# Optimization experiments

Measured on AMD Instinct MI355X. Metric: run time of the kernel, lower is better.

The kernel has to match this reference:

```python
import jax, jax.numpy as jnp
import numpy as np

EMBED_DIM = 1024
NUM_HEADS = 16
HEAD_DIM = EMBED_DIM // NUM_HEADS
B, T = 4, 1024
NEG = -1.0e9
LN_EPS = 1e-5


def setup_inputs() -> dict:
    key = jax.random.key(0)
    ks = jax.random.split(key, 13)
    s = 1.0 / np.sqrt(EMBED_DIM)
    return {
        "query": jax.random.normal(ks[0], (B, T, EMBED_DIM), jnp.float32),
        "key": jax.random.normal(ks[1], (B, T, EMBED_DIM), jnp.float32),
        "value": jax.random.normal(ks[2], (B, T, EMBED_DIM), jnp.float32),
        "mask": jax.random.randint(ks[3], (B, 1, T, T), 0, 2, jnp.int32),
        "Wq": jax.random.normal(ks[4], (EMBED_DIM, EMBED_DIM), jnp.float32) * s,
        "bq": jnp.zeros((EMBED_DIM,), jnp.float32),
        "Wk": jax.random.normal(ks[5], (EMBED_DIM, EMBED_DIM), jnp.float32) * s,
        "bk": jnp.zeros((EMBED_DIM,), jnp.float32),
        "Wv": jax.random.normal(ks[6], (EMBED_DIM, EMBED_DIM), jnp.float32) * s,
        "bv": jnp.zeros((EMBED_DIM,), jnp.float32),
        "Wo": jax.random.normal(ks[7], (EMBED_DIM, EMBED_DIM), jnp.float32) * s,
        "bo": jnp.zeros((EMBED_DIM,), jnp.float32),
        "gamma": jnp.ones((EMBED_DIM,), jnp.float32),
        "beta": jnp.zeros((EMBED_DIM,), jnp.float32),
    }


def _split_heads(x):
    # (B, T, E) -> (B, H, T, D)
    b, t, _ = x.shape
    return x.reshape(b, t, NUM_HEADS, HEAD_DIM).transpose(0, 2, 1, 3)


def _mha(query, key, value, mask, Wq, bq, Wk, bk, Wv, bv, Wo, bo, gamma, beta,
         temperature=1.0):
    q = _split_heads(query @ Wq.T + bq)
    k = _split_heads(key @ Wk.T + bk)
    v = _split_heads(value @ Wv.T + bv)
    # scores: (B, H, T, T)
    scale = jnp.sqrt(jnp.float32(HEAD_DIM)) * temperature
    scores = jnp.einsum("bhqd,bhkd->bhqk", q, k) / scale
    scores = jnp.where(mask == 0, NEG, scores)
    scores = scores - jnp.max(scores, axis=-1, keepdims=True)
    # temperature >= 0.01 in this config, so the low-temperature hard-cutoff
    # branch is skipped (matches torch's Python-level `if temperature < 0.01`).
    scores = jnp.nan_to_num(scores, nan=0.0, posinf=1.0e9, neginf=-1.0e9)
    attn = jax.nn.softmax(scores, axis=-1)
    # eval mode: dropout is identity (self.training is False)
    out = jnp.einsum("bhqk,bhkd->bhqd", attn, v)  # (B, H, T, D)
    out = out.transpose(0, 2, 1, 3).reshape(query.shape[0], query.shape[1], EMBED_DIM)
    out = out @ Wo.T + bo
    # layer norm over embed_dim
    mu = jnp.mean(out, axis=-1, keepdims=True)
    var = jnp.mean(jnp.square(out - mu), axis=-1, keepdims=True)
    out = (out - mu) * jax.lax.rsqrt(var + LN_EPS) * gamma + beta
    return out


def reference(query, key, value, mask, Wq, bq, Wk, bk, Wv, bv, Wo, bo, gamma, beta):
    return _mha(query, key, value, mask, Wq, bq, Wk, bk, Wv, bv, Wo, bo, gamma, beta)
```

## Files before the change

### kernel.cpp

```cpp
#include <hip/hip_runtime.h>
#include <cmath>

#define T_SEQ 1024
#define EMB   1024
#define NH    16
#define HD    64
#define NB    4
#define BQ    64
#define BK    64

#define QSCALE 0.18033688011112042f
#define BIAS2  -1.44269504e9f

using frag8   = __attribute__((ext_vector_type(8))) short;
using f32x4   = __attribute__((ext_vector_type(4))) float;
using short4v = __attribute__((ext_vector_type(4))) short;
using short8v = __attribute__((ext_vector_type(8))) short;

__device__ inline short f2bf(float f) {
    union { float f; unsigned u; } x; x.f = f;
    unsigned r = (x.u + 0x7FFFu + ((x.u >> 16) & 1u)) >> 16;
    return (short)r;
}
__device__ inline float bf2f(unsigned short u) {
    union { unsigned u; float f; } x; x.u = ((unsigned)u) << 16;
    return x.f;
}
__device__ inline int cvt_pk_bf16(float lo, float hi) {
    int r;
    asm("v_cvt_pk_bf16_f32 %0, %1, %2" : "=v"(r) : "v"(lo), "v"(hi));
    return r;
}

__device__ inline void glds16(const short* g, short* l) {
    __builtin_amdgcn_global_load_lds(
        (const __attribute__((address_space(1))) void*)g,
        (__attribute__((address_space(3))) void*)l, 16, 0, 0);
}

struct ConvArgs { const float* src[7]; short* dst[7]; int n8[7]; };

__global__ __launch_bounds__(256) void convert_bf16(ConvArgs a) {
    const int y = blockIdx.y;
    const int t = blockIdx.x * 256 + threadIdx.x;
    if (t >= a.n8[y]) return;
    const float4* s = (const float4*)a.src[y];
    const float4 v0 = s[t * 2], v1 = s[t * 2 + 1];
    short8v o;
    o[0] = f2bf(v0.x); o[1] = f2bf(v0.y); o[2] = f2bf(v0.z); o[3] = f2bf(v0.w);
    o[4] = f2bf(v1.x); o[5] = f2bf(v1.y); o[6] = f2bf(v1.z); o[7] = f2bf(v1.w);
    *(short8v*)&a.dst[y][t * 8] = o;
}

__global__ __launch_bounds__(256) void convert_mask(
    const int* __restrict__ mask, short* __restrict__ dst)
{
    const int wave = threadIdx.x >> 6, lane = threadIdx.x & 63;
    const int tile = blockIdx.x * 4 + wave;
    const int bb   = tile >> 12;
    const int q16  = (tile >> 6) & 63;
    const int k16  = tile & 63;
    const int qrow = lane >> 2;
    const int col4 = (lane & 3) * 4;
    const int4 mv = *(const int4*)&mask[((size_t)bb * T_SEQ + q16 * 16 + qrow) * T_SEQ
                                        + k16 * 16 + col4];
    const short BB = f2bf(BIAS2);
    short4v o;
    o[0] = mv.x ? (short)0 : BB;
    o[1] = mv.y ? (short)0 : BB;
    o[2] = mv.z ? (short)0 : BB;
    o[3] = mv.w ? (short)0 : BB;
    *(short4v*)&dst[(size_t)tile * 256 + qrow * 16 + col4] = o;
}

struct GemmB { const short* A; const short* W; const float* bias; short* out; float scale; };
struct QkvArgs { GemmB g[3]; };

template <int MODE>
__device__ inline void gemm_core(short* __restrict__ As,
                                 short* __restrict__ Bs,
                                 const short* __restrict__ A,
                                 const short* __restrict__ W,
                                 const float* __restrict__ bias,
                                 float scale,
                                 short* __restrict__ outS,
                                 float* __restrict__ outF,
                                 int m0, int n0)
{
    const int tid  = threadIdx.x;
    const int wave = tid >> 6;
    const int lane = tid & 63;
    const int quad = lane >> 4;
    const int lm   = lane & 15;
    const int wr   = wave >> 1;
    const int wc   = wave & 1;
    const int K    = EMB;

    const int G0 = wave * 64 + lane, G1 = G0 + 256;
    const short* aSrc0 = A + (size_t)(m0 + (G0 >> 2)) * K + (G0 & 3) * 8;
    const short* aSrc1 = A + (size_t)(m0 + (G1 >> 2)) * K + (G1 & 3) * 8;
    const short* bSrc0 = W + (size_t)(n0 + (G0 >> 2)) * K + (G0 & 3) * 8;
    const short* bSrc1 = W + (size_t)(n0 + (G1 >> 2)) * K + (G1 & 3) * 8;
    short* aDst0 = As + wave * 512;
    short* aDst1 = As + 2048 + wave * 512;
    short* bDst0 = Bs + wave * 512;
    short* bDst1 = Bs + 2048 + wave * 512;

    f32x4 acc[4][4];
#pragma unroll
    for (int i = 0; i < 4; ++i)
#pragma unroll
        for (int j = 0; j < 4; ++j) acc[i][j] = (f32x4){0.f, 0.f, 0.f, 0.f};

    for (int kk = 0; kk < K; kk += 64) {
        __syncthreads();
        glds16(aSrc0 + kk,      aDst0);
        glds16(aSrc1 + kk,      aDst1);
        glds16(bSrc0 + kk,      bDst0);
        glds16(bSrc1 + kk,      bDst1);
        glds16(aSrc0 + kk + 32, aDst0 + 4096);
        glds16(aSrc1 + kk + 32, aDst1 + 4096);
        glds16(bSrc0 + kk + 32, bDst0 + 4096);
        glds16(bSrc1 + kk + 32, bDst1 + 4096);
        __syncthreads();

#pragma unroll
        for (int p = 0; p < 2; ++p) {
            frag8 aF[4], bF[4];
#pragma unroll
            for (int i = 0; i < 4; ++i)
                aF[i] = *(const frag8*)&As[p * 4096 + (wr * 64 + i * 16 + lm) * 32 + quad * 8];
#pragma unroll
            for (int j = 0; j < 4; ++j)
                bF[j] = *(const frag8*)&Bs[p * 4096 + (wc * 64 + j * 16 + lm) * 32 + quad * 8];
#pragma unroll
            for (int i = 0; i < 4; ++i)
#pragma unroll
                for (int j = 0; j < 4; ++j)
                    acc[i][j] = __builtin_amdgcn_mfma_f32_16x16x32_bf16(
                        aF[i], bF[j], acc[i][j], 0, 0, 0);
        }
    }

#pragma unroll
    for (int i = 0; i < 4; ++i)
#pragma unroll
        for (int j = 0; j < 4; ++j) {
            const int n = n0 + wc * 64 + j * 16 + lm;
            const float bv = bias[n];
#pragma unroll
            for (int rr = 0; rr < 4; ++rr) {
                const int m = m0 + wr * 64 + i * 16 + quad * 4 + rr;
                const float val = (acc[i][j][rr] + bv) * scale;
                if (MODE == 0) {
                    outF[((size_t)(m >> 4) * 64 + (n >> 4)) * 256 +
                         rr * 64 + quad * 16 + lm] = val;
                } else {
                    const int bb = m >> 10, tt = m & 1023;
                    const int h = n >> 6,  d  = n & 63;
                    const size_t bh = (size_t)bb * NH + h;
                    if (MODE == 1) {
                        outS[((bh * 64 + (tt >> 4)) * 8 + (d >> 3)) * 128 +
                             (tt & 15) * 8 + (d & 7)] = f2bf(val);
                    } else {
                        outS[((((bh * 16 + (tt >> 6)) * 2 + ((tt >> 5) & 1)) * 4 +
                              (d >> 4)) * 4 + ((tt >> 2) & 3)) * 128 +
                             (d & 15) * 8 + (((tt & 16) >> 2) | (tt & 3))] = f2bf(val);
                    }
                }
            }
        }
}

__global__ __launch_bounds__(256, 4) void gemm_qkv(QkvArgs args) {
    __shared__ short As[2 * 128 * 32];
    __shared__ short Bs[2 * 128 * 32];
    const int id = blockIdx.x + 8 * blockIdx.y + 256 * blockIdx.z;
    const int a  = id & 7;
    const int k2 = id >> 3;
    const int nb = k2 & 7;
    const int c  = k2 >> 3;
    const int pair = a * 12 + c;
    const int mb = pair & 31;
    const int zb = pair >> 5;
    const GemmB g = args.g[zb];
    if (zb < 2) gemm_core<1>(As, Bs, g.A, g.W, g.bias, g.scale, g.out, nullptr, mb * 128, nb * 128);
    else        gemm_core<2>(As, Bs, g.A, g.W, g.bias, g.scale, g.out, nullptr, mb * 128, nb * 128);
}

__global__ __launch_bounds__(256, 4) void gemm_wo(const short* __restrict__ A,
                                                  const short* __restrict__ W,
                                                  const float* __restrict__ bias,
                                                  float* __restrict__ out) {
    __shared__ short As[2 * 128 * 32];
    __shared__ short Bs[2 * 128 * 32];
    const int id = blockIdx.x + 8 * blockIdx.y;
    const int a  = id & 7;
    const int k2 = id >> 3;
    const int nb = k2 & 7;
    const int c  = k2 >> 3;
    const int mb = a * 4 + c;
    gemm_core<0>(As, Bs, A, W, bias, 1.0f, nullptr, out, mb * 128, nb * 128);
}

__global__ __launch_bounds__(512, 4) void flash_attn_mfma(
    const short* __restrict__ qf_, const short* __restrict__ kf_,
    const short* __restrict__ vf_, const short* __restrict__ mf_,
    short* __restrict__ out)
{
    __shared__ short KV[4][4096];

    const int tid  = threadIdx.x;
    const int wave = tid >> 6;
    const int lane = tid & 63;
    const int quad = lane >> 4;
    const int lm   = lane & 15;
    const int wq   = wave & 3;
    const int wk   = wave >> 2;

    const int id  = blockIdx.x;
    const int xcd = id & 7;
    const int idx = id >> 3;
    const int bh_i = xcd * 8 + (idx >> 4);
    const int b  = bh_i >> 4, h = bh_i & 15;
    const int q0 = (idx & 15) * BQ;
    const size_t bh = (size_t)bh_i;

    const int  sbuf  = wave >> 1;
    const int  shalf = (wave & 1) * 2048;
    const short* sb = ((sbuf < 2) ? kf_ : vf_) + bh * 65536
                      + (size_t)(sbuf & 1) * 32768 + shalf + lane * 8;
    short* dstb = &KV[sbuf][shalf];

    const short* qb_ = qf_ + (bh * 64 + (q0 >> 4) + wq) * 1024;
    const frag8 qfa = *(const frag8*)&qb_[(quad * 16 + lm) * 8];
    const frag8 qfb = *(const frag8*)&qb_[((quad + 4) * 16 + lm) * 8];

    const short* mrow = mf_ + ((size_t)b * 64 + (q0 >> 4) + wq) * (64 * 256)
                        + lm * 16 + quad * 4;

    union { int i[4]; frag8 f; } ones;
    ones.i[0] = ones.i[1] = ones.i[2] = ones.i[3] = 0x3F803F80;

    f32x4 of[4];
#pragma unroll
    for (int dc = 0; dc < 4; ++dc) of[dc] = (f32x4){0.f, 0.f, 0.f, 0.f};
    f32x4 ls = (f32x4){0.f, 0.f, 0.f, 0.f};

    for (int kt = 0; kt < 8; ++kt) {
        const int kt2 = wk * 8 + kt;

        __syncthreads();
#pragma unroll
        for (int it = 0; it < 4; ++it)
            glds16(sb + kt * 4096 + it * 512, dstb + it * 512);

        short4v mb[4];
#pragma unroll
        for (int kc = 0; kc < 4; ++kc)
            mb[kc] = *(const short4v*)&mrow[(kt2 * 4 + kc) * 256];
        __syncthreads();

        f32x4 s[4];
#pragma unroll
        for (int kc = 0; kc < 4; ++kc) {
            const short* kb = &KV[wk][kc * 1024];
            const frag8 kfa = *(const frag8*)&kb[(quad * 16 + lm) * 8];
            const frag8 kfb = *(const frag8*)&kb[((quad + 4) * 16 + lm) * 8];
            f32x4 a = (f32x4){ bf2f((unsigned short)mb[kc][0]),
                               bf2f((unsigned short)mb[kc][1]),
                               bf2f((unsigned short)mb[kc][2]),
                               bf2f((unsigned short)mb[kc][3]) };
            a = __builtin_amdgcn_mfma_f32_16x16x32_bf16(kfa, qfa, a, 0, 0, 0);
            a = __builtin_amdgcn_mfma_f32_16x16x32_bf16(kfb, qfb, a, 0, 0, 0);
            s[kc] = a;
        }

#pragma unroll
        for (int kc = 0; kc < 4; ++kc) {
            s[kc][0] = exp2f(s[kc][0]); s[kc][1] = exp2f(s[kc][1]);
            s[kc][2] = exp2f(s[kc][2]); s[kc][3] = exp2f(s[kc][3]);
        }

        union { int i[4]; frag8 f; } ua, ub;
        ua.i[0] = cvt_pk_bf16(s[0][0], s[0][1]);
        ua.i[1] = cvt_pk_bf16(s[0][2], s[0][3]);
        ua.i[2] = cvt_pk_bf16(s[1][0], s[1][1]);
        ua.i[3] = cvt_pk_bf16(s[1][2], s[1][3]);
        ub.i[0] = cvt_pk_bf16(s[2][0], s[2][1]);
        ub.i[1] = cvt_pk_bf16(s[2][2], s[2][3]);
        ub.i[2] = cvt_pk_bf16(s[3][0], s[3][1]);
        ub.i[3] = cvt_pk_bf16(s[3][2], s[3][3]);

        __builtin_amdgcn_s_setprio(1);
#pragma unroll
        for (int dc = 0; dc < 4; ++dc) {
            const frag8 v0 = *(const frag8*)&KV[2 + wk][(dc * 4 + quad) * 128 + lm * 8];
            const frag8 v1 = *(const frag8*)&KV[2 + wk][((4 + dc) * 4 + quad) * 128 + lm * 8];
            of[dc] = __builtin_amdgcn_mfma_f32_16x16x32_bf16(v0, ua.f, of[dc], 0, 0, 0);
            of[dc] = __builtin_amdgcn_mfma_f32_16x16x32_bf16(v1, ub.f, of[dc], 0, 0, 0);
        }
        ls = __builtin_amdgcn_mfma_f32_16x16x32_bf16(ones.f, ua.f, ls, 0, 0, 0);
        ls = __builtin_amdgcn_mfma_f32_16x16x32_bf16(ones.f, ub.f, ls, 0, 0, 0);
        __builtin_amdgcn_s_setprio(0);
    }

    float* Osh = (float*)&KV[0][0];
    __syncthreads();
    if (wk) {
#pragma unroll
        for (int c = 0; c < 16; ++c) Osh[(wq * 17 + c) * 64 + lane] = of[c >> 2][c & 3];
        Osh[(wq * 17 + 16) * 64 + lane] = ls[0];
    }
    __syncthreads();
    if (!wk) {
#pragma unroll
        for (int c = 0; c < 16; ++c) of[c >> 2][c & 3] += Osh[(wq * 17 + c) * 64 + lane];
        const float lsum = ls[0] + Osh[(wq * 17 + 16) * 64 + lane];
        const float inv = 1.0f / lsum;

        short* ob = out + ((size_t)b * T_SEQ + q0 + wq * 16 + lm) * EMB + h * HD;
#pragma unroll
        for (int dc = 0; dc < 4; ++dc) {
            short4v o4;
#pragma unroll
            for (int rr = 0; rr < 4; ++rr) o4[rr] = f2bf(of[dc][rr] * inv);
            *(short4v*)&ob[dc * 16 + quad * 4] = o4;
        }
    }
}

__global__ __launch_bounds__(256) void layernorm_k(
    const float* __restrict__ x, const float* __restrict__ gamma,
    const float* __restrict__ beta, float* __restrict__ out)
{
    __shared__ float ws1[4], ws2[4];
    const int tid = threadIdx.x;
    const int row = blockIdx.x;
    const int m16 = row >> 4, rr = row & 3, qd = (row >> 2) & 3;

    const float4 v = *(const float4*)&x[((size_t)m16 * 64 + (tid >> 2)) * 256 +
                                        rr * 64 + qd * 16 + (tid & 3) * 4];
    float s  = v.x + v.y + v.z + v.w;
    float ss = v.x * v.x + v.y * v.y + v.z * v.z + v.w * v.w;
#pragma unroll
    for (int off = 32; off > 0; off >>= 1) {
        s  += __shfl_down(s, off);
        ss += __shfl_down(ss, off);
    }
    if ((tid & 63) == 0) { ws1[tid >> 6] = s; ws2[tid >> 6] = ss; }
    __syncthreads();
    if (tid == 0) {
        const float a = ws1[0] + ws1[1] + ws1[2] + ws1[3];
        const float bsum = ws2[0] + ws2[1] + ws2[2] + ws2[3];
        const float mu = a * (1.0f / EMB);
        const float var = bsum * (1.0f / EMB) - mu * mu;
        ws1[0] = mu;
        ws2[0] = rsqrtf(var + 1e-5f);
    }
    __syncthreads();
    const float mu = ws1[0], rstd = ws2[0];

    const float4 g = *(const float4*)&gamma[tid * 4];
    const float4 bt = *(const float4*)&beta[tid * 4];
    float4 r;
    r.x = (v.x - mu) * rstd * g.x + bt.x;
    r.y = (v.y - mu) * rstd * g.y + bt.y;
    r.z = (v.z - mu) * rstd * g.z + bt.z;
    r.w = (v.w - mu) * rstd * g.w + bt.w;
    *(float4*)&out[(size_t)row * EMB + tid * 4] = r;
}

extern "C" void kernel_launch(void* const* d_in, const int* in_sizes, int n_in,
                              void* d_out, int out_size, void* d_ws, size_t ws_size,
                              hipStream_t stream) {
    const float* query = (const float*)d_in[0];
    const float* key_i = (const float*)d_in[1];
    const float* value = (const float*)d_in[2];
    const int*   mask  = (const int*)d_in[3];
    const float* Wq = (const float*)d_in[4];
    const float* bq = (const float*)d_in[5];
    const float* Wk = (const float*)d_in[6];
    const float* bk = (const float*)d_in[7];
    const float* Wv = (const float*)d_in[8];
    const float* bv = (const float*)d_in[9];
    const float* Wo = (const float*)d_in[10];
    const float* bo = (const float*)d_in[11];
    const float* gamma = (const float*)d_in[12];
    const float* beta  = (const float*)d_in[13];

    const size_t SZ = (size_t)NB * T_SEQ * EMB;
    const size_t WZ = (size_t)EMB * EMB;
    short* sws = (short*)d_ws;
    short* q_bf  = sws;
    short* k_bf  = sws + SZ;
    short* v_bf  = sws + 2 * SZ;
    short* w_bf  = sws + 3 * SZ;
    short* qh    = sws + 4 * SZ;
    short* kh    = sws + 5 * SZ;
    short* vh    = sws + 6 * SZ;
    short* maskb = sws + 7 * SZ;
    short* attnb = q_bf;
    float* projb = (float*)(sws + SZ);

    ConvArgs ca;
    ca.src[0] = query; ca.dst[0] = q_bf;          ca.n8[0] = (int)(SZ / 8);
    ca.src[1] = key_i; ca.dst[1] = k_bf;          ca.n8[1] = (int)(SZ / 8);
    ca.src[2] = value; ca.dst[2] = v_bf;          ca.n8[2] = (int)(SZ / 8);
    ca.src[3] = Wq;    ca.dst[3] = w_bf;          ca.n8[3] = (int)(WZ / 8);
    ca.src[4] = Wk;    ca.dst[4] = w_bf + WZ;     ca.n8[4] = (int)(WZ / 8);
    ca.src[5] = Wv;    ca.dst[5] = w_bf + 2 * WZ; ca.n8[5] = (int)(WZ / 8);
    ca.src[6] = Wo;    ca.dst[6] = w_bf + 3 * WZ; ca.n8[6] = (int)(WZ / 8);
    convert_bf16<<<dim3((SZ / 8 + 255) / 256, 7), 256, 0, stream>>>(ca);

    convert_mask<<<dim3(NB * 64 * 64 / 4), 256, 0, stream>>>(mask, maskb);

    QkvArgs qa;
    qa.g[0] = { q_bf, w_bf,          bq, qh, QSCALE };
    qa.g[1] = { k_bf, w_bf + WZ,     bk, kh, 1.0f };
    qa.g[2] = { v_bf, w_bf + 2 * WZ, bv, vh, 1.0f };
    gemm_qkv<<<dim3(EMB / 128, NB * T_SEQ / 128, 3), 256, 0, stream>>>(qa);

    flash_attn_mfma<<<dim3(T_SEQ / BQ * NH * NB), 512, 0, stream>>>(qh, kh, vh, maskb, attnb);

    gemm_wo<<<dim3(EMB / 128, NB * T_SEQ / 128), 256, 0, stream>>>(
        attnb, w_bf + 3 * WZ, bo, projb);

    layernorm_k<<<dim3(NB * T_SEQ), 256, 0, stream>>>(projb, gamma, beta, (float*)d_out);
}
```

Measured before the change: 249.6 us.

## Double-buffer K/V shared tiles and prefetch mask in flash attention

New measurement: 244.1 us. 2.2% less time.

```diff
diff --git a/kernel.cpp b/kernel.cpp
--- a/kernel.cpp
+++ b/kernel.cpp
@@ -208,7 +208,7 @@
     const short* __restrict__ vf_, const short* __restrict__ mf_,
     short* __restrict__ out)
 {
-    __shared__ short KV[4][4096];
+    __shared__ short KV[2][4][4096];
 
     const int tid  = threadIdx.x;
     const int wave = tid >> 6;
@@ -230,7 +230,6 @@
     const int  shalf = (wave & 1) * 2048;
     const short* sb = ((sbuf < 2) ? kf_ : vf_) + bh * 65536
                       + (size_t)(sbuf & 1) * 32768 + shalf + lane * 8;
-    short* dstb = &KV[sbuf][shalf];
 
     const short* qb_ = qf_ + (bh * 64 + (q0 >> 4) + wq) * 1024;
     const frag8 qfa = *(const frag8*)&qb_[(quad * 16 + lm) * 8];
@@ -247,30 +246,43 @@
     for (int dc = 0; dc < 4; ++dc) of[dc] = (f32x4){0.f, 0.f, 0.f, 0.f};
     f32x4 ls = (f32x4){0.f, 0.f, 0.f, 0.f};
 
+#pragma unroll
+    for (int it = 0; it < 4; ++it)
+        glds16(sb + it * 512, &KV[0][sbuf][shalf + it * 512]);
+    short4v mb[4];
+#pragma unroll
+    for (int kc = 0; kc < 4; ++kc)
+        mb[kc] = *(const short4v*)&mrow[(wk * 32 + kc) * 256];
+    __syncthreads();
+
     for (int kt = 0; kt < 8; ++kt) {
-        const int kt2 = wk * 8 + kt;
-
-        __syncthreads();
-#pragma unroll
-        for (int it = 0; it < 4; ++it)
-            glds16(sb + kt * 4096 + it * 512, dstb + it * 512);
-
-        short4v mb[4];
-#pragma unroll
-        for (int kc = 0; kc < 4; ++kc)
-            mb[kc] = *(const short4v*)&mrow[(kt2 * 4 + kc) * 256];
-        __syncthreads();
+        const int cur = kt & 1;
+
+        if (kt < 7) {
+#pragma unroll
+            for (int it = 0; it < 4; ++it)
+                glds16(sb + (kt + 1) * 4096 + it * 512,
+                       &KV[cur ^ 1][sbuf][shalf + it * 512]);
+        }
+        short4v mc[4];
+#pragma unroll
+        for (int kc = 0; kc < 4; ++kc) mc[kc] = mb[kc];
+        if (kt < 7) {
+#pragma unroll
+            for (int kc = 0; kc < 4; ++kc)
+                mb[kc] = *(const short4v*)&mrow[((wk * 8 + kt + 1) * 4 + kc) * 256];
+        }
 
         f32x4 s[4];
 #pragma unroll
         for (int kc = 0; kc < 4; ++kc) {
-            const short* kb = &KV[wk][kc * 1024];
+            const short* kb = &KV[cur][wk][kc * 1024];
             const frag8 kfa = *(const frag8*)&kb[(quad * 16 + lm) * 8];
             const frag8 kfb = *(const frag8*)&kb[((quad + 4) * 16 + lm) * 8];
-            f32x4 a = (f32x4){ bf2f((unsigned short)mb[kc][0]),
-                               bf2f((unsigned short)mb[kc][1]),
-                               bf2f((unsigned short)mb[kc][2]),
-                               bf2f((unsigned short)mb[kc][3]) };
+            f32x4 a = (f32x4){ bf2f((unsigned short)mc[kc][0]),
+                               bf2f((unsigned short)mc[kc][1]),
+                               bf2f((unsigned short)mc[kc][2]),
+                               bf2f((unsigned short)mc[kc][3]) };
             a = __builtin_amdgcn_mfma_f32_16x16x32_bf16(kfa, qfa, a, 0, 0, 0);
             a = __builtin_amdgcn_mfma_f32_16x16x32_bf16(kfb, qfb, a, 0, 0, 0);
             s[kc] = a;
@@ -295,18 +307,19 @@
         __builtin_amdgcn_s_setprio(1);
 #pragma unroll
         for (int dc = 0; dc < 4; ++dc) {
-            const frag8 v0 = *(const frag8*)&KV[2 + wk][(dc * 4 + quad) * 128 + lm * 8];
-            const frag8 v1 = *(const frag8*)&KV[2 + wk][((4 + dc) * 4 + quad) * 128 + lm * 8];
+            const frag8 v0 = *(const frag8*)&KV[cur][2 + wk][(dc * 4 + quad) * 128 + lm * 8];
+            const frag8 v1 = *(const frag8*)&KV[cur][2 + wk][((4 + dc) * 4 + quad) * 128 + lm * 8];
             of[dc] = __builtin_amdgcn_mfma_f32_16x16x32_bf16(v0, ua.f, of[dc], 0, 0, 0);
             of[dc] = __builtin_amdgcn_mfma_f32_16x16x32_bf16(v1, ub.f, of[dc], 0, 0, 0);
         }
         ls = __builtin_amdgcn_mfma_f32_16x16x32_bf16(ones.f, ua.f, ls, 0, 0, 0);
         ls = __builtin_amdgcn_mfma_f32_16x16x32_bf16(ones.f, ub.f, ls, 0, 0, 0);
         __builtin_amdgcn_s_setprio(0);
-    }
-
-    float* Osh = (float*)&KV[0][0];
-    __syncthreads();
+
+        __syncthreads();
+    }
+
+    float* Osh = (float*)&KV[0][0][0];
     if (wk) {
 #pragma unroll
         for (int c = 0; c < 16; ++c) Osh[(wq * 17 + c) * 64 + lane] = of[c >> 2][c & 3];
```
